# Kernel optimization log

Measured on AMD Instinct MI355X. Metric: run time of the kernel, lower is better.

The kernel has to match this reference:

```python
import jax, jax.numpy as jnp
import numpy as np

N_FFT = 800
HOP = 200
WIN = 800
FREQ = N_FFT // 2 + 1  # 401
B, T = 32, 480000


def _make_weights():
    # periodic hann window
    n = np.arange(N_FFT)
    window = 0.5 - 0.5 * np.cos(2.0 * np.pi * np.arange(WIN) / WIN)
    k = np.arange(FREQ)
    angle = 2.0 * np.pi * np.outer(k, n) / N_FFT  # [FREQ, N_FFT]
    fwd_real = (np.cos(angle) * window).astype(np.float32)
    fwd_imag = (-np.sin(angle) * window).astype(np.float32)
    angle_t = 2.0 * np.pi * np.outer(n, k) / N_FFT  # [N_FFT, FREQ]
    inv_window = window * (1.0 / N_FFT)
    bwd_real = (np.cos(angle_t).T * inv_window).astype(np.float32)  # [FREQ, N_FFT]
    bwd_imag = (np.sin(angle_t).T * inv_window).astype(np.float32)
    return (jnp.asarray(fwd_real), jnp.asarray(fwd_imag),
            jnp.asarray(bwd_real), jnp.asarray(bwd_imag))


def setup_inputs() -> dict:
    key = jax.random.key(0)
    x = jax.random.normal(key, (B, T), dtype=jnp.float32)
    wfr, wfi, wbr, wbi = _make_weights()
    return {"x": x, "w_fwd_real": wfr, "w_fwd_imag": wfi,
            "w_bwd_real": wbr, "w_bwd_imag": wbi}


def reference(x, w_fwd_real, w_fwd_imag, w_bwd_real, w_bwd_imag):
    Tlen = x.shape[-1]
    pad = N_FFT // 2
    xp = jnp.pad(x, ((0, 0), (pad, pad)), mode="edge")  # replicate pad
    n_frames = (xp.shape[-1] - N_FFT) // HOP + 1
    # frame extraction (== conv1d stride HOP with dense DFT kernels)
    fidx = jnp.arange(n_frames)[:, None] * HOP + jnp.arange(N_FFT)[None, :]
    frames = xp[:, fidx]  # [B, F, N_FFT]
    real = jnp.einsum("bfn,kn->bkf", frames, w_fwd_real)  # [B, FREQ, F]
    imag = jnp.einsum("bfn,kn->bkf", frames, w_fwd_imag)
    magnitude = jnp.sqrt(real * real + imag * imag + 1e-14)
    phase = jnp.arctan2(imag, real)
    phase = jnp.where((imag == 0) & (real < 0), jnp.pi, phase)
    # inverse: iDFT-as-GEMM + overlap-add (== conv_transpose1d stride HOP)
    rp = magnitude * jnp.cos(phase)
    ip = magnitude * jnp.sin(phase)
    yr = jnp.einsum("bkf,kn->bfn", rp, w_bwd_real)  # [B, F, N_FFT]
    yi = jnp.einsum("bkf,kn->bfn", ip, w_bwd_imag)
    y_frames = yr - yi
    l_out = (n_frames - 1) * HOP + N_FFT
    oidx = jnp.arange(n_frames)[:, None] * HOP + jnp.arange(N_FFT)[None, :]
    wave = jnp.zeros((x.shape[0], l_out), dtype=x.dtype).at[:, oidx].add(y_frames)
    return wave[:, pad:pad + Tlen]
```

## Files before the change

### kernel.cpp

```cpp
#include <hip/hip_runtime.h>
#include <math.h>

#define HOP     200
#define NB      32
#define TLEN    480000
#define QPB     16
#define NQB     (TLEN / HOP / QPB)
#define NSEGP   22

#define DLT  0.00785398163397448f
#define C1K  0.99996915760f
#define S1K  0.00785390090f
#define C2K  0.99987663248f
#define S2K  0.01570731731f
#define C3K  0.99972243010f
#define S3K  0.02355976470f
#define C40  0.95105651629515f
#define S40  0.30901699437495f

__global__ __launch_bounds__(256) void stft_one(const float* __restrict__ x,
                                                float* __restrict__ out) {
    __shared__ float  part[NSEGP][10][6];
    __shared__ float  pg[NSEGP][6];
    __shared__ float4 segc[2][QPB];

    const int qb = blockIdx.x;
    const int b  = blockIdx.y;
    const int q0 = qb * QPB;
    const float* xb = x + (size_t)b * TLEN;

    if (threadIdx.x < NSEGP * 10) {
        const int s = threadIdx.x / 10;
        const int k = threadIdx.x - 10 * s;
        const int g = q0 - 3 + s;
        const int gm = (g + 4) & 3;
        float c0, s0;
        __sincosf((float)(gm * 200 + 4 * k) * DLT, &s0, &c0);
        float p1e = 0.f, p1o = 0.f, pce = 0.f, pco = 0.f, pse = 0.f, pso = 0.f;
        const bool inb = (g >= 0) && (g <= 2399);
        float4 ve;
        if (!inb) {
            const float xe = (g < 0) ? xb[0] : xb[TLEN - 1];
            ve = make_float4(xe, xe, xe, xe);
        }
#pragma unroll
        for (int i = 0; i < 5; ++i) {
            float4 v;
            if (inb) v = ((const float4*)(xb + 200 * g))[k + 10 * i];
            else     v = ve;
            const float c1 = c0 * C1K - s0 * S1K, s1 = s0 * C1K + c0 * S1K;
            const float c2 = c0 * C2K - s0 * S2K, s2 = s0 * C2K + c0 * S2K;
            const float c3 = c0 * C3K - s0 * S3K, s3 = s0 * C3K + c0 * S3K;
            p1e += v.x + v.z;            p1o += v.y + v.w;
            pce += c0 * v.x + c2 * v.z;  pco += c1 * v.y + c3 * v.w;
            pse += s0 * v.x + s2 * v.z;  pso += s1 * v.y + s3 * v.w;
            const float cn = c0 * C40 - s0 * S40;
            s0 = s0 * C40 + c0 * S40;  c0 = cn;
        }
        part[s][k][0] = p1e;  part[s][k][1] = p1o;
        part[s][k][2] = pce;  part[s][k][3] = pco;
        part[s][k][4] = pse;  part[s][k][5] = pso;
    }
    __syncthreads();

    if (threadIdx.x < NSEGP * 6) {
        const int s = threadIdx.x / 6;
        const int c = threadIdx.x - 6 * s;
        float a = 0.f;
#pragma unroll
        for (int k = 0; k < 10; ++k) a += part[s][k][c];
        pg[s][c] = a;
    }
    __syncthreads();

    if (threadIdx.x < 2 * QPB) {
        const int par = threadIdx.x & 1;
        const int ql  = threadIdx.x >> 1;
        const int q   = q0 + ql;
        float A = 0.f, C = 0.f, D = 0.f;
#pragma unroll
        for (int df = -1; df <= 2; ++df) {
            const int f = q + df;
            if (f < 0 || f > 2400) continue;
            const int ls0 = f - q0 + 1;
            float sp1 = 0.f, spc = 0.f, sps = 0.f;
#pragma unroll
            for (int kk = 0; kk < 4; ++kk) {
                const float* rec = pg[ls0 + kk];
                sp1 += rec[par];  spc += rec[2 + par];  sps += rec[4 + par];
            }
            const int fm = f & 3;
            const float tr = (fm == 0) ? spc : (fm == 1) ? sps : (fm == 2) ? -spc : -sps;
            const float S = 0.5f * sp1 + 0.5f * tr;
            A += S;
            if (fm == 0) C += S; else if (fm == 2) C -= S;
            else if (fm == 1) D += S; else D -= S;
        }
        segc[par][ql] = make_float4(A * (1.0f / 1600.0f),
                                    sqrtf(C * C + D * D) * (1.0f / 1600.0f),
                                    atan2f(D, C), 0.f);
    }
    __syncthreads();

    const bool headblk = (qb == 0);
    const bool tailblk = (qb == NQB - 1);
    const float4* xg4 = (const float4*)(xb + HOP * q0);
    float4* og4 = (float4*)(out + (size_t)b * TLEN + HOP * q0);
    const int pmb = (q0 & 3) * 200 + 400;
    for (int j = threadIdx.x; j < 50 * QPB; j += 256) {
        const float4 xv = xg4[j];
        const int sl = j / 50;
        const float4 ce = segc[0][sl];
        const float4 co = segc[1][sl];
        const int pm = (pmb + 4 * j) % 800;
        const float xa[4] = {xv.x, xv.y, xv.z, xv.w};
        float r[4];
#pragma unroll
        for (int c = 0; c < 4; ++c) {
            const float4 cc = (c & 1) ? co : ce;
            r[c] = 0.75f * xa[c] + cc.x - cc.y * __cosf((float)(pm + c) * DLT - cc.z);
        }
        if (headblk && sl == 0) {
#pragma unroll
            for (int c = 0; c < 4; ++c) {
                const float wm = 0.5f + 0.5f * __sinf((float)(pm + c) * DLT);
                r[c] -= 0.5f * wm * wm * xa[c];
            }
        }
        if (tailblk && sl == QPB - 1) {
#pragma unroll
            for (int c = 0; c < 4; ++c) {
                const float wm = 0.5f - 0.5f * __sinf((float)(pm + c) * DLT);
                r[c] -= 0.5f * wm * wm * xa[c];
            }
        }
        og4[j] = make_float4(r[0], r[1], r[2], r[3]);
    }
}

extern "C" void kernel_launch(void* const* d_in, const int* in_sizes, int n_in,
                              void* d_out, int out_size, void* d_ws, size_t ws_size,
                              hipStream_t stream) {
    const float* x = (const float*)d_in[0];
    float* out = (float*)d_out;
    stft_one<<<dim3(NQB, NB), dim3(256), 0, stream>>>(x, out);
}
```

Before: 122.7 us.

## Split segment partial sums into separate kernel to avoid redundant halo recomputation

The fused kernel is split into two. The first computes the per-segment partial DFT sums once per segment and writes them to a workspace buffer. The second kernel reads those 22 records per block instead of recomputing them, which removes the roughly 22/16 redundant halo work and its extra reads of x. The output stores also become nontemporal. The cost is an extra kernel launch and a small round trip through global memory.

Measured after the change: 124.5 us. No clear change (+1.5%).

```diff
diff --git a/kernel.cpp b/kernel.cpp
--- a/kernel.cpp
+++ b/kernel.cpp
@@ -4,9 +4,12 @@
 #define HOP     200
 #define NB      32
 #define TLEN    480000
+#define NSEGG   2404
 #define QPB     16
 #define NQB     (TLEN / HOP / QPB)
 #define NSEGP   22
+#define SEGPB   25
+#define NGB     ((NSEGG + SEGPB - 1) / SEGPB)
 
 #define DLT  0.00785398163397448f
 #define C1K  0.99996915760f
@@ -18,9 +21,70 @@
 #define C40  0.95105651629515f
 #define S40  0.30901699437495f
 
-__global__ __launch_bounds__(256) void stft_one(const float* __restrict__ x,
-                                                float* __restrict__ out) {
-    __shared__ float  part[NSEGP][10][6];
+typedef float floatx4 __attribute__((ext_vector_type(4)));
+
+
+__global__ __launch_bounds__(256) void seg_partials(const float* __restrict__ x,
+                                                    float* __restrict__ P) {
+    __shared__ float part[SEGPB][10][6];
+    const int b  = blockIdx.y;
+    const int s0 = blockIdx.x * SEGPB;
+    const float* xb = x + (size_t)b * TLEN;
+    const int t = threadIdx.x;
+
+    if (t < SEGPB * 10) {
+        const int s = t / 10;
+        const int k = t - 10 * s;
+        const int sg = s0 + s;
+        if (sg < NSEGG) {
+            const int g  = sg - 2;
+            const int gm = (g + 4) & 3;
+            float c0, sn0;
+            __sincosf((float)(gm * 200 + 4 * k) * DLT, &sn0, &c0);
+            float p1e = 0.f, p1o = 0.f, pce = 0.f, pco = 0.f, pse = 0.f, pso = 0.f;
+            const bool inb = (g >= 0) && (g <= 2399);
+            float4 ve;
+            if (!inb) {
+                const float xe = (g < 0) ? xb[0] : xb[TLEN - 1];
+                ve = make_float4(xe, xe, xe, xe);
+            }
+#pragma unroll
+            for (int i = 0; i < 5; ++i) {
+                float4 v;
+                if (inb) v = ((const float4*)(xb + 200 * g))[k + 10 * i];
+                else     v = ve;
+                const float c1 = c0 * C1K - sn0 * S1K, s1 = sn0 * C1K + c0 * S1K;
+                const float c2 = c0 * C2K - sn0 * S2K, s2 = sn0 * C2K + c0 * S2K;
+                const float c3 = c0 * C3K - sn0 * S3K, s3 = sn0 * C3K + c0 * S3K;
+                p1e += v.x + v.z;             p1o += v.y + v.w;
+                pce += c0 * v.x + c2 * v.z;   pco += c1 * v.y + c3 * v.w;
+                pse += sn0 * v.x + s2 * v.z;  pso += s1 * v.y + s3 * v.w;
+                const float cn = c0 * C40 - sn0 * S40;
+                sn0 = sn0 * C40 + c0 * S40;  c0 = cn;
+            }
+            part[s][k][0] = p1e;  part[s][k][1] = p1o;
+            part[s][k][2] = pce;  part[s][k][3] = pco;
+            part[s][k][4] = pse;  part[s][k][5] = pso;
+        }
+    }
+    __syncthreads();
+
+    if (t < SEGPB * 6) {
+        const int s = t / 6;
+        const int c = t - 6 * s;
+        const int sg = s0 + s;
+        if (sg < NSEGG) {
+            float a = 0.f;
+#pragma unroll
+            for (int k = 0; k < 10; ++k) a += part[s][k][c];
+            P[((size_t)b * NSEGG + sg) * 6 + c] = a;
+        }
+    }
+}
+
+__global__ __launch_bounds__(256) void synth(const float* __restrict__ x,
+                                             const float* __restrict__ P,
+                                             float* __restrict__ out) {
     __shared__ float  pg[NSEGP][6];
     __shared__ float4 segc[2][QPB];
 
@@ -29,47 +93,12 @@
     const int q0 = qb * QPB;
     const float* xb = x + (size_t)b * TLEN;
 
-    if (threadIdx.x < NSEGP * 10) {
-        const int s = threadIdx.x / 10;
-        const int k = threadIdx.x - 10 * s;
-        const int g = q0 - 3 + s;
-        const int gm = (g + 4) & 3;
-        float c0, s0;
-        __sincosf((float)(gm * 200 + 4 * k) * DLT, &s0, &c0);
-        float p1e = 0.f, p1o = 0.f, pce = 0.f, pco = 0.f, pse = 0.f, pso = 0.f;
-        const bool inb = (g >= 0) && (g <= 2399);
-        float4 ve;
-        if (!inb) {
-            const float xe = (g < 0) ? xb[0] : xb[TLEN - 1];
-            ve = make_float4(xe, xe, xe, xe);
-        }
-#pragma unroll
-        for (int i = 0; i < 5; ++i) {
-            float4 v;
-            if (inb) v = ((const float4*)(xb + 200 * g))[k + 10 * i];
-            else     v = ve;
-            const float c1 = c0 * C1K - s0 * S1K, s1 = s0 * C1K + c0 * S1K;
-            const float c2 = c0 * C2K - s0 * S2K, s2 = s0 * C2K + c0 * S2K;
-            const float c3 = c0 * C3K - s0 * S3K, s3 = s0 * C3K + c0 * S3K;
-            p1e += v.x + v.z;            p1o += v.y + v.w;
-            pce += c0 * v.x + c2 * v.z;  pco += c1 * v.y + c3 * v.w;
-            pse += s0 * v.x + s2 * v.z;  pso += s1 * v.y + s3 * v.w;
-            const float cn = c0 * C40 - s0 * S40;
-            s0 = s0 * C40 + c0 * S40;  c0 = cn;
-        }
-        part[s][k][0] = p1e;  part[s][k][1] = p1o;
-        part[s][k][2] = pce;  part[s][k][3] = pco;
-        part[s][k][4] = pse;  part[s][k][5] = pso;
-    }
-    __syncthreads();
-
     if (threadIdx.x < NSEGP * 6) {
-        const int s = threadIdx.x / 6;
-        const int c = threadIdx.x - 6 * s;
-        float a = 0.f;
-#pragma unroll
-        for (int k = 0; k < 10; ++k) a += part[s][k][c];
-        pg[s][c] = a;
+        const int sl = threadIdx.x / 6;
+        const int c  = threadIdx.x - 6 * sl;
+        int g = q0 - 3 + sl;
+        g = min(max(g, -2), 2401);
+        pg[sl][c] = P[((size_t)b * NSEGG + g + 2) * 6 + c];
     }
     __syncthreads();
 
@@ -105,7 +134,7 @@
     const bool headblk = (qb == 0);
     const bool tailblk = (qb == NQB - 1);
     const float4* xg4 = (const float4*)(xb + HOP * q0);
-    float4* og4 = (float4*)(out + (size_t)b * TLEN + HOP * q0);
+    floatx4* og4 = (floatx4*)(out + (size_t)b * TLEN + HOP * q0);
     const int pmb = (q0 & 3) * 200 + 400;
     for (int j = threadIdx.x; j < 50 * QPB; j += 256) {
         const float4 xv = xg4[j];
@@ -134,7 +163,8 @@
                 r[c] -= 0.5f * wm * wm * xa[c];
             }
         }
-        og4[j] = make_float4(r[0], r[1], r[2], r[3]);
+        floatx4 rv = {r[0], r[1], r[2], r[3]};
+        __builtin_nontemporal_store(rv, &og4[j]);
     }
 }
 
@@ -143,5 +173,8 @@
                               hipStream_t stream) {
     const float* x = (const float*)d_in[0];
     float* out = (float*)d_out;
-    stft_one<<<dim3(NQB, NB), dim3(256), 0, stream>>>(x, out);
+    float* P   = (float*)d_ws;
+
+    seg_partials<<<dim3(NGB, NB), dim3(256), 0, stream>>>(x, P);
+    synth<<<dim3(NQB, NB), dim3(256), 0, stream>>>(x, P, out);
 }
```
